# Kernel optimization log

Hardware: AMD Instinct MI355X
Metric: run time of the kernel (lower is better)

The kernel has to match this reference:

```python
import math
import jax, jax.numpy as jnp
import numpy as np

K_TOP = 8
D_HEAD = 32


def causal_topk_adjacency(x, K):
    # Binary adjacency: for each position t, top-K strictly-causal (j < t)
    # neighbours by dot-product similarity. Rows with < K valid positions
    # (e.g. t=0 has none) get only their valid entries (possibly zero rows).
    B, T, D = x.shape
    sim = jnp.einsum('btd,bsd->bts', x, x) / math.sqrt(D)  # (B,T,T)
    causal = jnp.tril(jnp.ones((T, T), dtype=bool), k=-1)   # j < t
    neg = jnp.finfo(sim.dtype).min
    sim_m = jnp.where(causal[None], sim, neg)
    vals, idx = jax.lax.top_k(sim_m, K)                      # (B,T,K)
    valid = (vals > neg).astype(x.dtype)
    b = jnp.arange(B)[:, None, None]
    t = jnp.arange(T)[None, :, None]
    A = jnp.zeros((B, T, T), x.dtype).at[b, t, idx].max(valid)
    return A


def setup_inputs() -> dict:
    key = jax.random.key(0)
    ks = jax.random.split(key, 3)
    B, T, D = 2, 4096, 1024
    x = jax.random.normal(ks[0], (B, T, D), dtype=jnp.float32)
    W_q = jax.random.normal(ks[1], (D_HEAD, D), dtype=jnp.float32) * (1.0 / math.sqrt(D))
    W_k = jax.random.normal(ks[2], (D_HEAD, D), dtype=jnp.float32) * (1.0 / math.sqrt(D))
    gain = jnp.ones((D,), dtype=jnp.float32)
    bias = jnp.zeros((D,), dtype=jnp.float32)
    log_mix = jnp.zeros((), dtype=jnp.float32)
    log_scale = jnp.zeros((), dtype=jnp.float32)
    return {"x": x, "W_q": W_q, "W_k": W_k, "gain": gain, "bias": bias,
            "log_mix": log_mix, "log_scale": log_scale}


def reference(x, W_q, W_k, gain, bias, log_mix, log_scale):
    B, T, D = x.shape
    mix = jax.nn.sigmoid(log_mix)
    scale = jax.nn.softplus(log_scale) + 0.01

    A = causal_topk_adjacency(x, K_TOP)                      # (B,T,T) binary

    q = jnp.einsum('btd,hd->bth', x, W_q)                    # (B,T,Dh)
    k = jnp.einsum('bsd,hd->bsh', x, W_k)
    score = jnp.einsum('bth,bsh->bts', q, k) / math.sqrt(D_HEAD)
    score = jnp.where(A < 0.5, -1e9, score)

    row_max = jax.lax.stop_gradient(jnp.max(score, axis=-1, keepdims=True))
    score = score - row_max
    attn = jax.nn.softmax(score, axis=-1)
    attn = jnp.nan_to_num(attn, nan=0.0)

    msg = jnp.einsum('bts,bsd->btd', attn, x)
    blended = mix * x + (1.0 - mix) * msg
    delta = jax.nn.gelu(blended * gain + bias, approximate=False) * scale
    return delta
```

## Files before the change

kernel.cpp:

```cpp
#include <hip/hip_runtime.h>
#include <math.h>

#define B 2
#define T 4096
#define D 1024
#define DH 32
#define TNB 32
#define NBLK 528
#define NK 12
#define CPR (32*NK)

typedef __bf16 bf16x8 __attribute__((ext_vector_type(8)));
typedef float f32x4 __attribute__((ext_vector_type(4)));
typedef unsigned u32x4 __attribute__((ext_vector_type(4)));

#define AS1 __attribute__((address_space(1)))
#define AS3 __attribute__((address_space(3)))

__device__ __forceinline__ unsigned mono32(float v) {
    unsigned u = __float_as_uint(v);
    u ^= ((unsigned)((int)u >> 31)) | 0x80000000u;
    return u;
}

__device__ __forceinline__ unsigned dpp_umax_bcast(unsigned v) {
    #define DPPMAX(CTRL) { unsigned t_ = (unsigned)__builtin_amdgcn_update_dpp(0, (int)v, CTRL, 0xF, 0xF, true); v = v > t_ ? v : t_; }
    DPPMAX(0x111) DPPMAX(0x112) DPPMAX(0x114) DPPMAX(0x118)
    DPPMAX(0x142) DPPMAX(0x143)
    #undef DPPMAX
    return (unsigned)__builtin_amdgcn_readlane((int)v, 63);
}
__device__ __forceinline__ float dpp_fsum_bcast(float v) {
    #define DPPADD(CTRL) { int t_ = __builtin_amdgcn_update_dpp(0, __float_as_int(v), CTRL, 0xF, 0xF, true); v += __int_as_float(t_); }
    DPPADD(0x111) DPPADD(0x112) DPPADD(0x114) DPPADD(0x118)
    DPPADD(0x142) DPPADD(0x143)
    #undef DPPADD
    return __int_as_float(__builtin_amdgcn_readlane(__float_as_int(v), 63));
}
__device__ __forceinline__ float dpp_gsum8(float p) {
    { int t_ = __builtin_amdgcn_update_dpp(0, __float_as_int(p), 0x0B1, 0xF, 0xF, true); p += __int_as_float(t_); }
    { int t_ = __builtin_amdgcn_update_dpp(0, __float_as_int(p), 0x04E, 0xF, 0xF, true); p += __int_as_float(t_); }
    { int t_ = __builtin_amdgcn_update_dpp(0, __float_as_int(p), 0x141, 0xF, 0xF, true); p += __int_as_float(t_); }
    return p;
}

__device__ __forceinline__ void merge12(const unsigned* a12, const unsigned* b12,
                                        unsigned* o12) {
    unsigned m16[16];
    #pragma unroll
    for (int i = 0; i < 16; ++i) {
        unsigned aa = (i < NK) ? a12[i] : 0u;
        unsigned bb = (15 - i < NK) ? b12[15 - i] : 0u;
        m16[i] = aa > bb ? aa : bb;
    }
    #pragma unroll
    for (int g = 8; g >= 1; g >>= 1) {
        #pragma unroll
        for (int i = 0; i < 16; ++i) {
            if (!(i & g)) {
                unsigned x0 = m16[i], x1 = m16[i + g];
                m16[i]     = x0 > x1 ? x0 : x1;
                m16[i + g] = x0 > x1 ? x1 : x0;
            }
        }
    }
    #pragma unroll
    for (int i = 0; i < NK; ++i) o12[i] = m16[i];
}

__device__ __forceinline__ void conv_body(const float* __restrict__ src,
        __bf16* __restrict__ dhi, __bf16* __restrict__ dlo, int i)
{
    float4 a = *(const float4*)(src + i);
    float4 c = *(const float4*)(src + i + 4);
    float av[8] = {a.x, a.y, a.z, a.w, c.x, c.y, c.z, c.w};
    __bf16 h[8], l[8];
    #pragma unroll
    for (int j = 0; j < 8; ++j) {
        h[j] = (__bf16)av[j];
        l[j] = (__bf16)(av[j] - (float)h[j]);
    }
    *(float4*)(dhi + i) = *(float4*)h;
    *(float4*)(dlo + i) = *(float4*)l;
}

__global__ __launch_bounds__(256) void prep_kernel(const float* __restrict__ x,
        const float* __restrict__ Wq, const float* __restrict__ Wk,
        __bf16* __restrict__ xhi, __bf16* __restrict__ xlo,
        __bf16* __restrict__ Whi, __bf16* __restrict__ Wlo,
        float* __restrict__ meansum2)
{
    int g = blockIdx.x;
    if (g < 4096) {
        conv_body(x, xhi, xlo, (g * 256 + threadIdx.x) << 3);
    } else if (g < 4128) {
        int gw = g - 4096;
        const float* src = (gw < 16) ? Wq : Wk;
        __bf16* dhi = Whi + ((gw < 16) ? 0 : 32 * D);
        __bf16* dlo = Wlo + ((gw < 16) ? 0 : 32 * D);
        conv_body(src, dhi, dlo, ((gw & 15) * 256 + threadIdx.x) << 3);
    } else {
        int gm = g - 4128;
        int b = gm >> 6;
        int rem = gm & 63;
        int dblk = rem >> 4;
        int tch = rem & 15;
        int d = dblk * 256 + threadIdx.x;
        const float* xp = x + (b * T + tch * 256) * D + d;
        float s = 0.f;
        #pragma unroll 8
        for (int it = 0; it < 256; ++it) s += xp[it * D];
        meansum2[(((b << 4) + tch) << 10) + d] = s;
    }
}

__global__ __launch_bounds__(256, 4) void qk_topk_kernel(
        const __bf16* __restrict__ xhi, const __bf16* __restrict__ xlo,
        const __bf16* __restrict__ Whi, const __bf16* __restrict__ Wlo,
        float* __restrict__ qo, float* __restrict__ ko,
        unsigned* __restrict__ pkey)
{
    __shared__ __align__(16) char smem[40960];
    int tid = threadIdx.x;
    int w = tid >> 6, lane = tid & 63;
    int fr = lane & 15, fq = lane >> 4;

    if (blockIdx.x < 128) {
        __bf16* sAhi = (__bf16*)smem;
        __bf16* sAlo = sAhi + 2560;
        __bf16* sBhi = sAhi + 5120;
        __bf16* sBlo = sAhi + 7680;

        int m0 = blockIdx.x << 6;
        int arow = tid >> 2, aq = tid & 3;
        const __bf16* gAh = xhi + (size_t)(m0 + arow) * D + aq * 8;
        const __bf16* gAl = xlo + (size_t)(m0 + arow) * D + aq * 8;
        const __bf16* gBh = Whi + arow * D + aq * 8;
        const __bf16* gBl = Wlo + arow * D + aq * 8;

        f32x4 acc[4];
        #pragma unroll
        for (int j = 0; j < 4; ++j) acc[j] = (f32x4){0.f, 0.f, 0.f, 0.f};

        float4 a0 = *(const float4*)(gAh);
        float4 a1 = *(const float4*)(gAl);
        float4 b0 = *(const float4*)(gBh);
        float4 b1 = *(const float4*)(gBl);

        int sa = arow * 40 + aq * 8;

        for (int kc = 0; kc < 32; ++kc) {
            __syncthreads();
            *(float4*)(sAhi + sa) = a0;
            *(float4*)(sAlo + sa) = a1;
            *(float4*)(sBhi + sa) = b0;
            *(float4*)(sBlo + sa) = b1;
            __syncthreads();
            if (kc + 1 < 32) {
                int k0 = (kc + 1) << 5;
                a0 = *(const float4*)(gAh + k0);
                a1 = *(const float4*)(gAl + k0);
                b0 = *(const float4*)(gBh + k0);
                b1 = *(const float4*)(gBl + k0);
            }
            int r = (w << 4) + fr;
            bf16x8 fah = *(const bf16x8*)(sAhi + r * 40 + fq * 8);
            bf16x8 fal = *(const bf16x8*)(sAlo + r * 40 + fq * 8);
            bf16x8 fbh[4], fbl[4];
            #pragma unroll
            for (int j = 0; j < 4; ++j) {
                int rb = j * 16 + fr;
                fbh[j] = *(const bf16x8*)(sBhi + rb * 40 + fq * 8);
                fbl[j] = *(const bf16x8*)(sBlo + rb * 40 + fq * 8);
            }
            #pragma unroll
            for (int j = 0; j < 4; ++j) {
                acc[j] = __builtin_amdgcn_mfma_f32_16x16x32_bf16(fah, fbh[j], acc[j], 0, 0, 0);
                acc[j] = __builtin_amdgcn_mfma_f32_16x16x32_bf16(fah, fbl[j], acc[j], 0, 0, 0);
                acc[j] = __builtin_amdgcn_mfma_f32_16x16x32_bf16(fal, fbh[j], acc[j], 0, 0, 0);
            }
        }
        int grow0 = m0 + (w << 4) + (fq << 2);
        #pragma unroll
        for (int j = 0; j < 4; ++j) {
            int gn = j * 16 + fr;
            float* dst = (gn < 32) ? (qo + grow0 * DH + gn)
                                   : (ko + grow0 * DH + gn - 32);
            dst[0]      = acc[j][0];
            dst[DH]     = acc[j][1];
            dst[2 * DH] = acc[j][2];
            dst[3 * DH] = acc[j][3];
        }
        return;
    }

    __bf16* stg = (__bf16*)smem;
    float* Sbuf = (float*)smem;

    int p = blockIdx.x - 128;
    int swz = (p & 7) * 132 + (p >> 3);
    int b = swz / NBLK;
    int l = swz - b * NBLK;
    int rt = (int)((sqrtf(8.f * l + 1.f) - 1.f) * 0.5f);
    while ((rt + 1) * (rt + 2) / 2 <= l) ++rt;
    while (rt * (rt + 1) / 2 > l) --rt;
    int ct = l - rt * (rt + 1) / 2;
    int r0 = rt << 7, c0 = ct << 7;
    int base = b * T;

    int wr = (w >> 1) << 6, wc = (w & 1) << 6;
    bool active = !(rt == ct && w == 1);
    int fqs = (fq ^ ((fr >> 1) & 3)) << 3;

    int lrow = lane >> 2;
    int lcq = (((lane & 3) ^ ((lane >> 3) & 3)) << 3);
    const __bf16* gA = xhi + (size_t)(base + r0) * D;
    const __bf16* gB = xhi + (size_t)(base + c0) * D;
    const __bf16* gA0 = gA + (size_t)((w << 4) + lrow) * D + lcq;
    const __bf16* gA1 = gA0 + (size_t)64 * D;
    const __bf16* gB0 = gB + (size_t)((w << 4) + lrow) * D + lcq;
    const __bf16* gB1 = gB0 + (size_t)64 * D;

    f32x4 acc[4][4];
    #pragma unroll
    for (int i = 0; i < 4; ++i)
        #pragma unroll
        for (int j = 0; j < 4; ++j) acc[i][j] = (f32x4){0.f, 0.f, 0.f, 0.f};

#define ISSUE_A(BUFBASE, KO) do { \
    __bf16* bA_ = (BUFBASE); \
    __builtin_amdgcn_global_load_lds((const AS1 unsigned int*)(gA0 + (KO)), \
        (AS3 unsigned int*)(bA_ + (w << 9)), 16, 0, 0); \
    __builtin_amdgcn_global_load_lds((const AS1 unsigned int*)(gA1 + (KO)), \
        (AS3 unsigned int*)(bA_ + 2048 + (w << 9)), 16, 0, 0); \
} while (0)
#define ISSUE_B(BUFBASE, KO) do { \
    __bf16* bB_ = (BUFBASE); \
    __builtin_amdgcn_global_load_lds((const AS1 unsigned int*)(gB0 + (KO)), \
        (AS3 unsigned int*)(bB_ + (w << 9)), 16, 0, 0); \
    __builtin_amdgcn_global_load_lds((const AS1 unsigned int*)(gB1 + (KO)), \
        (AS3 unsigned int*)(bB_ + 2048 + (w << 9)), 16, 0, 0); \
} while (0)

    ISSUE_B(stg + 12288, 0);
    ISSUE_A(stg, 0);
    ISSUE_A(stg + 4096, 32);

    int asel = 0, isel = 2;
    for (int kc = 0; kc < 32; ++kc) {
        if (kc < 31) { asm volatile("s_waitcnt vmcnt(2)" ::: "memory"); }
        else         { asm volatile("s_waitcnt vmcnt(0)" ::: "memory"); }
        __builtin_amdgcn_s_barrier();
        asm volatile("" ::: "memory");
        if (kc + 1 < 32)
            ISSUE_B(stg + 12288 + (((kc + 1) & 1) << 12), (kc + 1) << 5);
        if (kc + 2 < 32) {
            ISSUE_A(stg + (isel << 12), (kc + 2) << 5);
            isel = (isel == 2) ? 0 : isel + 1;
        }
        if (active) {
            const __bf16* cA = stg + (asel << 12);
            const __bf16* cB = stg + 12288 + ((kc & 1) << 12);
            bf16x8 ah[4], bh[4];
            #pragma unroll
            for (int i = 0; i < 4; ++i) {
                int ar = wr + i * 16 + fr;
                ah[i] = *(const bf16x8*)(cA + ar * 32 + fqs);
                int bc = wc + i * 16 + fr;
                bh[i] = *(const bf16x8*)(cB + bc * 32 + fqs);
            }
            #pragma unroll
            for (int i = 0; i < 4; ++i)
                #pragma unroll
                for (int j = 0; j < 4; ++j)
                    acc[i][j] = __builtin_amdgcn_mfma_f32_16x16x32_bf16(ah[i], bh[j], acc[i][j], 0, 0, 0);
        }
        asel = (asel == 2) ? 0 : asel + 1;
    }
#undef ISSUE_A
#undef ISSUE_B

    int cr = fq << 2, cc = fr;
    int q = lane >> 4;
    #pragma unroll
    for (int phase = 0; phase < 2; ++phase) {
        __syncthreads();
        if ((w >> 1) == phase) {
            #pragma unroll
            for (int i = 0; i < 4; ++i)
                #pragma unroll
                for (int j = 0; j < 4; ++j) {
                    float* sp = Sbuf + (i * 16 + cr) * 129 + wc + j * 16 + cc;
                    sp[0]       = acc[i][j][0];
                    sp[129]     = acc[i][j][1];
                    sp[2 * 129] = acc[i][j][2];
                    sp[3 * 129] = acc[i][j][3];
                }
        }
        __syncthreads();
        {
            int sr = (w << 4) + (lane & 15);
            int gt = r0 + (phase << 6) + sr;
            int cmax = gt - c0;
            if (cmax > 128) cmax = 128;
            if (cmax < 0) cmax = 0;
            int h0 = q << 5;
            int hmax = cmax < (h0 + 32) ? cmax : (h0 + 32);
            unsigned key[NK];
            #pragma unroll
            for (int i = 0; i < NK; ++i) key[i] = 0u;
            const float* Srow = Sbuf + sr * 129;
            #pragma unroll
            for (int mb = 0; mb < 4; ++mb) {
                int cb = h0 + (((mb + q) & 3) << 3);
                float v[8];
                #pragma unroll
                for (int j = 0; j < 8; ++j) v[j] = Srow[cb + j];
                #pragma unroll
                for (int j = 0; j < 8; ++j) {
                    int c = cb + j;
                    unsigned u = mono32(v[j]);
                    unsigned tk = (c < hmax) ? ((u & 0xFFFFFF80u) | (unsigned)(127 - c)) : 0u;
                    #pragma unroll
                    for (int i = 0; i < NK; ++i) {
                        unsigned hi = key[i] > tk ? key[i] : tk;
                        unsigned lo = key[i] > tk ? tk : key[i];
                        key[i] = hi; tk = lo;
                    }
                }
            }
            #pragma unroll
            for (int lvl = 0; lvl < 2; ++lvl) {
                int xm = 16 << lvl;
                unsigned o12[NK], m12[NK];
                #pragma unroll
                for (int i = 0; i < NK; ++i) o12[i] = __shfl_xor(key[i], xm);
                merge12(key, o12, m12);
                #pragma unroll
                for (int i = 0; i < NK; ++i) key[i] = m12[i];
            }
            if (q < 3) {
                u32x4 ov;
                #pragma unroll
                for (int j = 0; j < 4; ++j) {
                    unsigned k0 = (q == 0) ? key[j] : (q == 1) ? key[4 + j] : key[8 + j];
                    ov[j] = k0 ? ((k0 & 0xFFFFF000u) | ((k0 & 127u) + (unsigned)(3968 - c0))) : 0u;
                }
                *(u32x4*)(pkey + (size_t)(base + gt) * CPR + ct * NK + (q << 2)) = ov;
            }
        }
    }
}

__global__ __launch_bounds__(256) void select_msg_kernel(const float* __restrict__ x,
        const float* __restrict__ q, const float* __restrict__ k,
        const float* __restrict__ meansum2,
        const unsigned* __restrict__ pkey,
        const float* __restrict__ gain, const float* __restrict__ bias,
        const float* __restrict__ plm, const float* __restrict__ pls,
        float* __restrict__ out)
{
    int tid = threadIdx.x;
    int w = tid >> 6, lane = tid & 63;
    int rid = (blockIdx.x << 2) + w;
    int b = rid >> 12, t = rid & (T - 1);
    int ncand = NK * ((t + 127) >> 7);

    unsigned cv[6];
    #pragma unroll
    for (int u = 0; u < 6; ++u) {
        int cid = lane + (u << 6);
        cv[u] = (cid < ncand) ? pkey[(size_t)rid * CPR + cid] : 0u;
    }
    const float* xt = x + (size_t)rid * D;
    float4 xt4[4];
    #pragma unroll
    for (int c = 0; c < 4; ++c)
        xt4[c] = *(const float4*)(xt + (c << 8) + (lane << 2));

    unsigned skey[NK]; int sgid[NK];
    #pragma unroll
    for (int i = 0; i < NK; ++i) {
        unsigned m = cv[0];
        #pragma unroll
        for (int u = 1; u < 6; ++u) m = m > cv[u] ? m : cv[u];
        m = dpp_umax_bcast(m);
        skey[i] = m;
        sgid[i] = 4095 - (int)(m & 4095u);
        #pragma unroll
        for (int u = 0; u < 6; ++u) cv[u] = (cv[u] == m) ? 0u : cv[u];
    }

    float ex[NK];
    #pragma unroll
    for (int batch = 0; batch < 3; ++batch) {
        float4 rv[4][4];
        #pragma unroll
        for (int s = 0; s < 4; ++s) {
            int i = batch * 4 + s;
            int row = (skey[i] != 0u) ? sgid[i] : 0;
            const float* xj = x + (size_t)((b << 12) + row) * D;
            #pragma unroll
            for (int c = 0; c < 4; ++c)
                rv[s][c] = *(const float4*)(xj + (c << 8) + (lane << 2));
        }
        #pragma unroll
        for (int s = 0; s < 4; ++s) {
            float ss = 0.f;
            #pragma unroll
            for (int c = 0; c < 4; ++c)
                ss += xt4[c].x * rv[s][c].x + xt4[c].y * rv[s][c].y
                    + xt4[c].z * rv[s][c].z + xt4[c].w * rv[s][c].w;
            ex[batch * 4 + s] = dpp_fsum_bcast(ss);
        }
    }

    unsigned long long top8[8];
    #pragma unroll
    for (int r = 0; r < 8; ++r) top8[r] = 0ull;
    #pragma unroll
    for (int i = 0; i < NK; ++i) {
        unsigned u = mono32(ex[i]);
        unsigned long long t64 = (skey[i] != 0u)
            ? ((((unsigned long long)u) << 12) | (unsigned long long)(4095 - sgid[i]))
            : 0ull;
        #pragma unroll
        for (int r = 0; r < 8; ++r) {
            unsigned long long hi = (t64 > top8[r]) ? t64 : top8[r];
            unsigned long long lo = (t64 > top8[r]) ? top8[r] : t64;
            top8[r] = hi; t64 = lo;
        }
    }
    bool vld[8]; int bidx[8];
    #pragma unroll
    for (int i = 0; i < 8; ++i) {
        vld[i]  = top8[i] != 0ull;
        bidx[i] = 4095 - (int)(top8[i] & 4095ull);
    }

    int i8 = lane >> 3, e = lane & 7;
    unsigned long long kk = (i8 & 4)
        ? ((i8 & 2) ? ((i8 & 1) ? top8[7] : top8[6]) : ((i8 & 1) ? top8[5] : top8[4]))
        : ((i8 & 2) ? ((i8 & 1) ? top8[3] : top8[2]) : ((i8 & 1) ? top8[1] : top8[0]));
    bool v8 = kk != 0ull;
    int g8 = v8 ? (4095 - (int)(kk & 4095ull)) : 0;
    float4 qv = *(const float4*)(q + (size_t)rid * DH + (e << 2));
    float4 kv = *(const float4*)(k + (size_t)((b << 12) + g8) * DH + (e << 2));
    float p = qv.x * kv.x + qv.y * kv.y + qv.z * kv.z + qv.w * kv.w;
    p = dpp_gsum8(p);
    p *= 0.17677669529663687f;

    float sc[8];
    #pragma unroll
    for (int i = 0; i < 8; ++i)
        sc[i] = __int_as_float(__builtin_amdgcn_readlane(__float_as_int(p), i << 3));

    float m = -INFINITY; int cnt = 0;
    #pragma unroll
    for (int i = 0; i < 8; ++i)
        if (vld[i]) { ++cnt; if (sc[i] > m) m = sc[i]; }

    float wgt[8]; float Z = 0.f; int gsel[8];
    #pragma unroll
    for (int i = 0; i < 8; ++i) {
        wgt[i] = vld[i] ? expf(sc[i] - m) : 0.f;
        Z += wgt[i];
        gsel[i] = vld[i] ? ((b << 12) + bidx[i]) : (b << 12);
    }
    float invZ = (cnt > 0) ? 1.f / Z : 0.f;
    #pragma unroll
    for (int i = 0; i < 8; ++i) wgt[i] *= invZ;

    float mix   = 1.f / (1.f + expf(-plm[0]));
    float scale = log1pf(expf(pls[0])) + 0.01f;
    const float onemix = 1.f - mix;

    float4 msg4[4];
    if (cnt == 0) {
        #pragma unroll
        for (int c = 0; c < 4; ++c) {
            int d0 = (c << 8) + (lane << 2);
            float4 a4 = (float4){0.f, 0.f, 0.f, 0.f};
            #pragma unroll
            for (int tch = 0; tch < 16; ++tch) {
                float4 ms = *(const float4*)(meansum2 + (((b << 4) + tch) << 10) + d0);
                a4.x += ms.x; a4.y += ms.y; a4.z += ms.z; a4.w += ms.w;
            }
            msg4[c].x = a4.x * (1.f / (float)T); msg4[c].y = a4.y * (1.f / (float)T);
            msg4[c].z = a4.z * (1.f / (float)T); msg4[c].w = a4.w * (1.f / (float)T);
        }
    } else {
        #pragma unroll
        for (int c = 0; c < 4; ++c) msg4[c] = (float4){0.f, 0.f, 0.f, 0.f};
        #pragma unroll
        for (int g = 0; g < 2; ++g) {
            float4 rv[4][4];
            #pragma unroll
            for (int s = 0; s < 4; ++s) {
                const float* xj = x + (size_t)gsel[g * 4 + s] * D;
                #pragma unroll
                for (int c = 0; c < 4; ++c)
                    rv[s][c] = *(const float4*)(xj + (c << 8) + (lane << 2));
            }
            #pragma unroll
            for (int s = 0; s < 4; ++s) {
                float wi = wgt[g * 4 + s];
                #pragma unroll
                for (int c = 0; c < 4; ++c) {
                    msg4[c].x += wi * rv[s][c].x; msg4[c].y += wi * rv[s][c].y;
                    msg4[c].z += wi * rv[s][c].z; msg4[c].w += wi * rv[s][c].w;
                }
            }
        }
    }
    #pragma unroll
    for (int c = 0; c < 4; ++c) {
        int d0 = (c << 8) + (lane << 2);
        float4 g4 = *(const float4*)(gain + d0);
        float4 b4 = *(const float4*)(bias + d0);
        float4 xv = xt4[c];
        float zi[4] = {
            (mix * xv.x + onemix * msg4[c].x) * g4.x + b4.x,
            (mix * xv.y + onemix * msg4[c].y) * g4.y + b4.y,
            (mix * xv.z + onemix * msg4[c].z) * g4.z + b4.z,
            (mix * xv.w + onemix * msg4[c].w) * g4.w + b4.w };
        float4 o4;
        o4.x = 0.5f * zi[0] * (1.f + erff(zi[0] * 0.70710678118654752f)) * scale;
        o4.y = 0.5f * zi[1] * (1.f + erff(zi[1] * 0.70710678118654752f)) * scale;
        o4.z = 0.5f * zi[2] * (1.f + erff(zi[2] * 0.70710678118654752f)) * scale;
        o4.w = 0.5f * zi[3] * (1.f + erff(zi[3] * 0.70710678118654752f)) * scale;
        *(float4*)(out + (size_t)rid * D + d0) = o4;
    }
}

extern "C" void kernel_launch(void* const* d_in, const int* in_sizes, int n_in,
                              void* d_out, int out_size, void* d_ws, size_t ws_size,
                              hipStream_t stream)
{
    const float* x    = (const float*)d_in[0];
    const float* Wq   = (const float*)d_in[1];
    const float* Wk   = (const float*)d_in[2];
    const float* gain = (const float*)d_in[3];
    const float* bias = (const float*)d_in[4];
    const float* plm  = (const float*)d_in[5];
    const float* pls  = (const float*)d_in[6];
    float* out = (float*)d_out;

    float* ws       = (float*)d_ws;
    float* q        = ws;
    float* k        = ws + 262144;
    float* meansum2 = ws + 524288;
    unsigned* pkey  = (unsigned*)(ws + 557056);
    __bf16* xhi     = (__bf16*)(ws + 3702784);
    __bf16* xlo     = xhi + (size_t)B * T * D;
    __bf16* Whi     = xlo + (size_t)B * T * D;
    __bf16* Wlo     = Whi + 64 * D;

    prep_kernel<<<4256, 256, 0, stream>>>(x, Wq, Wk, xhi, xlo, Whi, Wlo, meansum2);
    qk_topk_kernel<<<128 + B * NBLK, 256, 0, stream>>>(xhi, xlo, Whi, Wlo, q, k, pkey);
    select_msg_kernel<<<B * T / 4, 256, 0, stream>>>(x, q, k, meansum2, pkey,
                                                     gain, bias, plm, pls, out);
}
```

Before: 233.4 us.

## Stage similarity tile as bf16 in LDS and select candidates in one pass

The 128x128 similarity tile is now written to shared memory as bf16 with stride 130, not fp32 in two 64-row phases, so the whole tile fits at once and one barrier pair is removed. Each row is scanned by two half-wave lanes over 64 columns each with 16-byte vector loads, which needs one shuffle-merge level instead of two, and one lane writes all three output chunks. Rounding scores to bf16 before ranking can change tie order or near-tie candidate choice relative to the fp32 keys. Each lane also runs twice as many sorting-network steps, since only two lanes now share a row.

```diff
diff --git a/kernel.cpp b/kernel.cpp
--- a/kernel.cpp
+++ b/kernel.cpp
@@ -195,7 +195,7 @@
     }
 
     __bf16* stg = (__bf16*)smem;
-    float* Sbuf = (float*)smem;
+    __bf16* Sb  = (__bf16*)smem;
 
     int p = blockIdx.x - 128;
     int swz = (p & 7) * 132 + (p >> 3);
@@ -280,73 +280,71 @@
 #undef ISSUE_A
 #undef ISSUE_B
 
-    int cr = fq << 2, cc = fr;
-    int q = lane >> 4;
-    #pragma unroll
-    for (int phase = 0; phase < 2; ++phase) {
-        __syncthreads();
-        if ((w >> 1) == phase) {
-            #pragma unroll
-            for (int i = 0; i < 4; ++i)
+    __syncthreads();
+    {
+        int cr = fq << 2;
+        #pragma unroll
+        for (int i = 0; i < 4; ++i) {
+            int R0 = wr + i * 16 + cr;
+            #pragma unroll
+            for (int j = 0; j < 4; ++j) {
+                int C = wc + j * 16 + fr;
                 #pragma unroll
-                for (int j = 0; j < 4; ++j) {
-                    float* sp = Sbuf + (i * 16 + cr) * 129 + wc + j * 16 + cc;
-                    sp[0]       = acc[i][j][0];
-                    sp[129]     = acc[i][j][1];
-                    sp[2 * 129] = acc[i][j][2];
-                    sp[3 * 129] = acc[i][j][3];
+                for (int r = 0; r < 4; ++r)
+                    Sb[(R0 + r) * 130 + C] = (__bf16)acc[i][j][r];
+            }
+        }
+    }
+    __syncthreads();
+    {
+        int srow = (w << 5) + (lane & 31);
+        int half = lane >> 5;
+        int gt = r0 + srow;
+        int cmax = gt - c0;
+        if (cmax > 128) cmax = 128;
+        if (cmax < 0) cmax = 0;
+        int h0 = half << 6;
+        int hmax = cmax < (h0 + 64) ? cmax : (h0 + 64);
+        unsigned key[NK];
+        #pragma unroll
+        for (int i = 0; i < NK; ++i) key[i] = 0u;
+        const __bf16* Srow = Sb + srow * 130;
+        #pragma unroll
+        for (int mb = 0; mb < 8; ++mb) {
+            int cb = h0 + (mb << 3);
+            bf16x8 v8 = *(const bf16x8*)(Srow + cb);
+            #pragma unroll
+            for (int j = 0; j < 8; ++j) {
+                int c = cb + j;
+                unsigned u = mono32((float)v8[j]);
+                unsigned tk = (c < hmax) ? ((u & 0xFFFFFF80u) | (unsigned)(127 - c)) : 0u;
+                #pragma unroll
+                for (int i = 0; i < NK; ++i) {
+                    unsigned hi = key[i] > tk ? key[i] : tk;
+                    unsigned lo = key[i] > tk ? tk : key[i];
+                    key[i] = hi; tk = lo;
                 }
-        }
-        __syncthreads();
+            }
+        }
         {
-            int sr = (w << 4) + (lane & 15);
-            int gt = r0 + (phase << 6) + sr;
-            int cmax = gt - c0;
-            if (cmax > 128) cmax = 128;
-            if (cmax < 0) cmax = 0;
-            int h0 = q << 5;
-            int hmax = cmax < (h0 + 32) ? cmax : (h0 + 32);
-            unsigned key[NK];
-            #pragma unroll
-            for (int i = 0; i < NK; ++i) key[i] = 0u;
-            const float* Srow = Sbuf + sr * 129;
-            #pragma unroll
-            for (int mb = 0; mb < 4; ++mb) {
-                int cb = h0 + (((mb + q) & 3) << 3);
-                float v[8];
-                #pragma unroll
-                for (int j = 0; j < 8; ++j) v[j] = Srow[cb + j];
-                #pragma unroll
-                for (int j = 0; j < 8; ++j) {
-                    int c = cb + j;
-                    unsigned u = mono32(v[j]);
-                    unsigned tk = (c < hmax) ? ((u & 0xFFFFFF80u) | (unsigned)(127 - c)) : 0u;
-                    #pragma unroll
-                    for (int i = 0; i < NK; ++i) {
-                        unsigned hi = key[i] > tk ? key[i] : tk;
-                        unsigned lo = key[i] > tk ? tk : key[i];
-                        key[i] = hi; tk = lo;
-                    }
-                }
-            }
-            #pragma unroll
-            for (int lvl = 0; lvl < 2; ++lvl) {
-                int xm = 16 << lvl;
-                unsigned o12[NK], m12[NK];
-                #pragma unroll
-                for (int i = 0; i < NK; ++i) o12[i] = __shfl_xor(key[i], xm);
-                merge12(key, o12, m12);
-                #pragma unroll
-                for (int i = 0; i < NK; ++i) key[i] = m12[i];
-            }
-            if (q < 3) {
+            unsigned o12[NK], m12[NK];
+            #pragma unroll
+            for (int i = 0; i < NK; ++i) o12[i] = __shfl_xor(key[i], 32);
+            merge12(key, o12, m12);
+            #pragma unroll
+            for (int i = 0; i < NK; ++i) key[i] = m12[i];
+        }
+        if (half == 0) {
+            int ob = (base + gt) * CPR + ct * NK;
+            #pragma unroll
+            for (int part = 0; part < 3; ++part) {
                 u32x4 ov;
                 #pragma unroll
                 for (int j = 0; j < 4; ++j) {
-                    unsigned k0 = (q == 0) ? key[j] : (q == 1) ? key[4 + j] : key[8 + j];
+                    unsigned k0 = key[part * 4 + j];
                     ov[j] = k0 ? ((k0 & 0xFFFFF000u) | ((k0 & 127u) + (unsigned)(3968 - c0))) : 0u;
                 }
-                *(u32x4*)(pkey + (size_t)(base + gt) * CPR + ct * NK + (q << 2)) = ov;
+                *(u32x4*)(pkey + ob + (part << 2)) = ov;
             }
         }
     }
```

Measured after the change: 231.0 us. No clear change (-1.0%).
